# Kernel tuning notes

Measured on AMD Instinct MI355X. Metric: run time of the kernel, lower is better.

The kernel has to match this reference:

```python
import jax, jax.numpy as jnp
import numpy as np

N_NODES = 100000
N_EDGES = 1600000
IN_DIM, HID, OUT = 256, 128, 32


def setup_inputs() -> dict:
    key = jax.random.key(0)
    ks = jax.random.split(key, 8)
    x = jax.random.normal(ks[0], (N_NODES, IN_DIM), dtype=jnp.float32)
    edge_index = jax.random.randint(ks[1], (2, N_EDGES), 0, N_NODES, dtype=jnp.int64)
    # Glorot-ish small scale to keep activations stable
    W0 = jax.random.normal(ks[2], (IN_DIM, HID), dtype=jnp.float32) * 0.05
    W1 = jax.random.normal(ks[3], (HID, HID), dtype=jnp.float32) * 0.05
    W2 = jax.random.normal(ks[4], (HID, OUT), dtype=jnp.float32) * 0.05
    b0 = jnp.zeros((HID,), jnp.float32)
    b1 = jnp.zeros((HID,), jnp.float32)
    b2 = jnp.zeros((OUT,), jnp.float32)
    return {"x": x, "edge_index": edge_index, "W0": W0, "b0": b0,
            "W1": W1, "b1": b1, "W2": W2, "b2": b2}


def reference(x, edge_index, W0, b0, W1, b1, W2, b2):
    # PyG GCNConv: add self-loops, symmetric normalization D^-1/2 A D^-1/2,
    # messages flow src (row 0) -> dst (row 1), aggregated at dst.
    n = x.shape[0]
    src, dst = edge_index[0], edge_index[1]
    ones = jnp.ones((src.shape[0],), x.dtype)
    deg = jax.ops.segment_sum(ones, dst, num_segments=n) + 1.0  # +1 for self-loop
    dinv = jax.lax.rsqrt(deg)                                   # [N]
    edge_norm = dinv[src] * dinv[dst]                           # [E]
    self_norm = dinv * dinv                                     # [N] self-loop weight

    def gcn_conv(h, W, b):
        h = h @ W                                               # [N, D_out]
        agg = jax.ops.segment_sum(h[src] * edge_norm[:, None], dst, num_segments=n)
        return agg + h * self_norm[:, None] + b

    h = gcn_conv(x, W0, b0)
    # dropout after layers i != 0: identity in eval mode (deterministic reference)
    h = gcn_conv(h, W1, b1)
    h = gcn_conv(h, W2, b2)
    return jax.nn.log_softmax(h, axis=1)
```

## Files before the change

kernel.cpp:

```cpp
#include <hip/hip_runtime.h>
#include <hip/hip_bf16.h>
#include <type_traits>

#define N_NODES 100000
#define N_EDGES 1600000
#define SLICE_N 12500
#define CAP     64

typedef float f32x4 __attribute__((ext_vector_type(4)));
typedef _Float16 f16x8 __attribute__((ext_vector_type(8)));
typedef _Float16 f16x4 __attribute__((ext_vector_type(4)));

__global__ __launch_bounds__(256) void fill_bucket_kernel(const int* __restrict__ esrc,
                                                          const int* __restrict__ edst,
                                                          int* __restrict__ cnt,
                                                          int* __restrict__ esorted) {
    const int slice = blockIdx.x & 7;
    const int chunk = blockIdx.x >> 3;
    const int base = chunk * 2048 + threadIdx.x;
    const int lo = slice * SLICE_N, hi = lo + SLICE_N;
    #pragma unroll
    for (int i = 0; i < 8; ++i) {
        int e = base + i * 256;
        if (e < N_EDGES) {
            int d = edst[e];
            if (d >= lo && d < hi) {
                int pos = atomicAdd(&cnt[d], 1);
                if (pos < CAP) esorted[(size_t)d * CAP + pos] = esrc[e];
            }
        }
    }
}

__global__ void dinv_kernel(const int* __restrict__ cnt, float* __restrict__ dinv) {
    int i = blockIdx.x * 256 + threadIdx.x;
    if (i < N_NODES) dinv[i] = 1.0f / sqrtf((float)cnt[i] + 1.0f);
}

__global__ void wconv_all_kernel(const float* __restrict__ W0, const float* __restrict__ W1,
                                 const float* __restrict__ W2, _Float16* __restrict__ Wt0,
                                 _Float16* __restrict__ Wt1, _Float16* __restrict__ Wt2) {
    int i = blockIdx.x * 256 + threadIdx.x;
    if (i < 32768) {
        int k = i / 128, col = i % 128;
        Wt0[col * 256 + k] = (_Float16)W0[i];
    } else if (i < 49152) {
        int j = i - 32768;
        int k = j / 128, col = j % 128;
        Wt1[col * 128 + k] = (_Float16)W1[j];
    } else if (i < 53248) {
        int j = i - 49152;
        int k = j / 32, col = j % 32;
        Wt2[col * 128 + k] = (_Float16)W2[j];
    }
}

#define LOADA(st, k0)                                                          \
    do {                                                                       \
        _Pragma("unroll")                                                      \
        for (int r = 0; r < 2; ++r) {                                          \
            const AT* ap = A + (size_t)gr[r] * K + (k0) + kof;                 \
            if constexpr (AF32) {                                              \
                a32[st][r][0] = *(const f32x4*)ap;                             \
                a32[st][r][1] = *(const f32x4*)(ap + 4);                       \
            } else {                                                           \
                a16[st][r] = *(const f16x8*)ap;                                \
            }                                                                  \
        }                                                                      \
    } while (0)

#define LOADB(st, k0)                                                          \
    do {                                                                       \
        _Pragma("unroll")                                                      \
        for (int c = 0; c < FC; ++c)                                           \
            bst[st][c] = *(const f16x8*)(Bt + (size_t)(c * 16 + l15) * K + (k0) + kof); \
    } while (0)

template<int K, int M, typename AT>
__global__ __launch_bounds__(256) void mfma_gemm_f16(const AT* __restrict__ A,
                                                     const _Float16* __restrict__ Bt,
                                                     const float* __restrict__ dinv,
                                                     _Float16* __restrict__ C) {
    constexpr bool AF32 = std::is_same<AT, float>::value;
    constexpr int FC = M / 16;
    constexpr int NIT = K / 32;
    const int tid = threadIdx.x;
    const int wave = tid >> 6, lane = tid & 63;
    const int row0 = blockIdx.x * 128;
    const int r0 = wave * 32;
    const int l15 = lane & 15, kof = (lane >> 4) * 8;

    f32x4 acc[2][FC] = {};
    int gr[2];
    #pragma unroll
    for (int r = 0; r < 2; ++r) {
        int g = row0 + r0 + r * 16 + l15;
        gr[r] = (g < N_NODES) ? g : N_NODES - 1;
    }

    f32x4 a32[3][2][2];
    f16x8 a16[3][2];
    f16x8 bst[2][FC];

    LOADA(0, 0);
    if (NIT > 1) LOADA(1, 32);
    LOADB(0, 0);

    #pragma unroll
    for (int it = 0; it < NIT; ++it) {
        if (it + 2 < NIT) LOADA((it + 2) % 3, (it + 2) * 32);
        if (it + 1 < NIT) LOADB((it + 1) % 2, (it + 1) * 32);
        f16x8 af[2];
        #pragma unroll
        for (int r = 0; r < 2; ++r) {
            if constexpr (AF32) {
                #pragma unroll
                for (int j = 0; j < 4; ++j) {
                    af[r][j] = (_Float16)a32[it % 3][r][0][j];
                    af[r][4 + j] = (_Float16)a32[it % 3][r][1][j];
                }
            } else {
                af[r] = a16[it % 3][r];
            }
        }
        #pragma unroll
        for (int c = 0; c < FC; ++c)
            #pragma unroll
            for (int r = 0; r < 2; ++r)
                acc[r][c] = __builtin_amdgcn_mfma_f32_16x16x32_f16(af[r], bst[it % 2][c], acc[r][c], 0, 0, 0);
    }

    #pragma unroll
    for (int r = 0; r < 2; ++r) {
        #pragma unroll
        for (int j = 0; j < 4; ++j) {
            int g = row0 + r0 + r * 16 + (lane >> 4) * 4 + j;
            if (g >= N_NODES) continue;
            float s = dinv[g];
            #pragma unroll
            for (int c = 0; c < FC; ++c)
                C[(size_t)g * M + c * 16 + l15] = (_Float16)(acc[r][c][j] * s);
        }
    }
}

template<int M, int G>
__global__ __launch_bounds__(256) void gather_kernel(const int* __restrict__ cnt,
                                                     const int* __restrict__ esorted,
                                                     const float* __restrict__ dinv,
                                                     const f16x8* __restrict__ hs,
                                                     const float* __restrict__ bias,
                                                     _Float16* __restrict__ out) {
    static_assert(M == 8 * G, "layout");
    constexpr int R = M / 8;
    int gid = blockIdx.x * blockDim.x + threadIdx.x;
    int node = gid / G;
    int lane = gid % G;
    if (node >= N_NODES) return;
    int len = cnt[node]; if (len > CAP) len = CAP;
    const int* __restrict__ lst = esorted + (size_t)node * CAP;
    float dn = dinv[node];
    f16x8 hv = hs[(size_t)node * R + lane];
    float acc[8];
    #pragma unroll
    for (int d = 0; d < 8; ++d) acc[d] = (float)hv[d];
    int j = 0;
    for (; j + 8 <= len; j += 8) {
        int s[8];
        f16x8 v[8];
        #pragma unroll
        for (int k = 0; k < 8; ++k) s[k] = lst[j + k];
        #pragma unroll
        for (int k = 0; k < 8; ++k) v[k] = hs[(size_t)s[k] * R + lane];
        #pragma unroll
        for (int k = 0; k < 8; ++k)
            #pragma unroll
            for (int d = 0; d < 8; ++d) acc[d] += (float)v[k][d];
    }
    for (; j < len; ++j) {
        f16x8 v = hs[(size_t)lst[j] * R + lane];
        #pragma unroll
        for (int d = 0; d < 8; ++d) acc[d] += (float)v[d];
    }
    const float* bp = bias + lane * 8;
    f16x8 o;
    #pragma unroll
    for (int d = 0; d < 8; ++d) o[d] = (_Float16)(acc[d] * dn + bp[d]);
    *((f16x8*)out + (size_t)node * R + lane) = o;
}

__global__ __launch_bounds__(256) void gather_lsm_kernel(const int* __restrict__ cnt,
                                                         const int* __restrict__ esorted,
                                                         const float* __restrict__ dinv,
                                                         const f16x8* __restrict__ hs,
                                                         const float* __restrict__ bias,
                                                         float* __restrict__ out) {
    constexpr int R = 4;
    int gid = blockIdx.x * blockDim.x + threadIdx.x;
    int node = gid / 4;
    int lane = gid % 4;
    if (node >= N_NODES) return;
    int len = cnt[node]; if (len > CAP) len = CAP;
    const int* __restrict__ lst = esorted + (size_t)node * CAP;
    float dn = dinv[node];
    f16x8 hv = hs[(size_t)node * R + lane];
    float acc[8];
    #pragma unroll
    for (int d = 0; d < 8; ++d) acc[d] = (float)hv[d];
    int j = 0;
    for (; j + 8 <= len; j += 8) {
        int s[8];
        f16x8 v[8];
        #pragma unroll
        for (int k = 0; k < 8; ++k) s[k] = lst[j + k];
        #pragma unroll
        for (int k = 0; k < 8; ++k) v[k] = hs[(size_t)s[k] * R + lane];
        #pragma unroll
        for (int k = 0; k < 8; ++k)
            #pragma unroll
            for (int d = 0; d < 8; ++d) acc[d] += (float)v[k][d];
    }
    for (; j < len; ++j) {
        f16x8 v = hs[(size_t)lst[j] * R + lane];
        #pragma unroll
        for (int d = 0; d < 8; ++d) acc[d] += (float)v[d];
    }
    const float* bp = bias + lane * 8;
    float o[8];
    #pragma unroll
    for (int d = 0; d < 8; ++d) o[d] = acc[d] * dn + bp[d];
    float m = o[0];
    #pragma unroll
    for (int d = 1; d < 8; ++d) m = fmaxf(m, o[d]);
    m = fmaxf(m, __shfl_xor(m, 1, 4));
    m = fmaxf(m, __shfl_xor(m, 2, 4));
    float s = 0.f;
    #pragma unroll
    for (int d = 0; d < 8; ++d) s += expf(o[d] - m);
    s += __shfl_xor(s, 1, 4);
    s += __shfl_xor(s, 2, 4);
    float ls = m + logf(s);
    f32x4 r0, r1;
    #pragma unroll
    for (int d = 0; d < 4; ++d) { r0[d] = o[d] - ls; r1[d] = o[4 + d] - ls; }
    f32x4* op = (f32x4*)out + (size_t)node * 8 + lane * 2;
    op[0] = r0;
    op[1] = r1;
}

extern "C" void kernel_launch(void* const* d_in, const int* in_sizes, int n_in,
                              void* d_out, int out_size, void* d_ws, size_t ws_size,
                              hipStream_t stream) {
    const float* x  = (const float*)d_in[0];
    const int*   ei = (const int*)d_in[1];
    const float* W0 = (const float*)d_in[2];
    const float* b0 = (const float*)d_in[3];
    const float* W1 = (const float*)d_in[4];
    const float* b1 = (const float*)d_in[5];
    const float* W2 = (const float*)d_in[6];
    const float* b2 = (const float*)d_in[7];
    float* out = (float*)d_out;

    char* ws = (char*)d_ws;
    float* dinv    = (float*)(ws + 0);
    int*   cnt     = (int*)  (ws + (512 << 10));
    int*   esorted = (int*)  (ws + (1 << 20));
    _Float16* Wt0  = (_Float16*)(ws + 27262976);
    _Float16* Wt1  = (_Float16*)(ws + 27262976 + 65536);
    _Float16* Wt2  = (_Float16*)(ws + 27262976 + 98304);
    _Float16* hs     = (_Float16*)(ws + 28311552);
    _Float16* bufB16 = (_Float16*)(ws + 28311552 + 26214400);
    const int* esrc = ei;
    const int* edst = ei + N_EDGES;

    const int NB = (N_NODES + 255) / 256;

    (void)hipMemsetAsync(cnt, 0, N_NODES * sizeof(int), stream);
    {
        const int chunks = (N_EDGES + 2047) / 2048;
        fill_bucket_kernel<<<chunks * 8, 256, 0, stream>>>(esrc, edst, cnt, esorted);
    }
    dinv_kernel<<<NB, 256, 0, stream>>>(cnt, dinv);
    wconv_all_kernel<<<208, 256, 0, stream>>>(W0, W1, W2, Wt0, Wt1, Wt2);

    const int RB128 = (N_NODES + 127) / 128;

    mfma_gemm_f16<256, 128, float><<<RB128, 256, 0, stream>>>(x, Wt0, dinv, hs);
    gather_kernel<128, 16><<<(N_NODES * 16 + 255) / 256, 256, 0, stream>>>(
        cnt, esorted, dinv, (const f16x8*)hs, b0, bufB16);

    mfma_gemm_f16<128, 128, _Float16><<<RB128, 256, 0, stream>>>(bufB16, Wt1, dinv, hs);
    gather_kernel<128, 16><<<(N_NODES * 16 + 255) / 256, 256, 0, stream>>>(
        cnt, esorted, dinv, (const f16x8*)hs, b1, bufB16);

    mfma_gemm_f16<128, 32, _Float16><<<RB128, 256, 0, stream>>>(bufB16, Wt2, dinv, hs);
    gather_lsm_kernel<<<(N_NODES * 4 + 255) / 256, 256, 0, stream>>>(
        cnt, esorted, dinv, (const f16x8*)hs, b2, out);
}
```

Measured before the change: 336.7 us.

## Co-schedule edge bucketing with first GEMM in one launch, defer dinv scaling

The edge-bucketing fill and the first layer's GEMM now run in a single launch, with one GEMM block interleaved among every eight fill blocks. The goal is to overlap the atomic-heavy, latency-bound bucketing with the bandwidth-bound x·W0 multiply. Because the degree counts are not final while the GEMM runs, the GEMM writes unscaled output. A new kernel then computes dinv and rescales hs in place, which replaces the old dinv kernel. The cost is an extra full read and write of the fp16 hidden buffer, plus added rounding from scaling after the fp16 store.

New measurement: 330.7 us. No clear change (-1.8%).

```diff
diff --git a/kernel.cpp b/kernel.cpp
--- a/kernel.cpp
+++ b/kernel.cpp
@@ -10,32 +10,6 @@
 typedef float f32x4 __attribute__((ext_vector_type(4)));
 typedef _Float16 f16x8 __attribute__((ext_vector_type(8)));
 typedef _Float16 f16x4 __attribute__((ext_vector_type(4)));
-
-__global__ __launch_bounds__(256) void fill_bucket_kernel(const int* __restrict__ esrc,
-                                                          const int* __restrict__ edst,
-                                                          int* __restrict__ cnt,
-                                                          int* __restrict__ esorted) {
-    const int slice = blockIdx.x & 7;
-    const int chunk = blockIdx.x >> 3;
-    const int base = chunk * 2048 + threadIdx.x;
-    const int lo = slice * SLICE_N, hi = lo + SLICE_N;
-    #pragma unroll
-    for (int i = 0; i < 8; ++i) {
-        int e = base + i * 256;
-        if (e < N_EDGES) {
-            int d = edst[e];
-            if (d >= lo && d < hi) {
-                int pos = atomicAdd(&cnt[d], 1);
-                if (pos < CAP) esorted[(size_t)d * CAP + pos] = esrc[e];
-            }
-        }
-    }
-}
-
-__global__ void dinv_kernel(const int* __restrict__ cnt, float* __restrict__ dinv) {
-    int i = blockIdx.x * 256 + threadIdx.x;
-    if (i < N_NODES) dinv[i] = 1.0f / sqrtf((float)cnt[i] + 1.0f);
-}
 
 __global__ void wconv_all_kernel(const float* __restrict__ W0, const float* __restrict__ W1,
                                  const float* __restrict__ W2, _Float16* __restrict__ Wt0,
@@ -76,17 +50,17 @@
             bst[st][c] = *(const f16x8*)(Bt + (size_t)(c * 16 + l15) * K + (k0) + kof); \
     } while (0)
 
-template<int K, int M, typename AT>
-__global__ __launch_bounds__(256) void mfma_gemm_f16(const AT* __restrict__ A,
-                                                     const _Float16* __restrict__ Bt,
-                                                     const float* __restrict__ dinv,
-                                                     _Float16* __restrict__ C) {
+template<int K, int M, typename AT, bool SCALE>
+__device__ __forceinline__ void gemm_tile_body(const AT* __restrict__ A,
+                                               const _Float16* __restrict__ Bt,
+                                               const float* __restrict__ dinv,
+                                               _Float16* __restrict__ C,
+                                               int blk, int tid) {
     constexpr bool AF32 = std::is_same<AT, float>::value;
     constexpr int FC = M / 16;
     constexpr int NIT = K / 32;
-    const int tid = threadIdx.x;
     const int wave = tid >> 6, lane = tid & 63;
-    const int row0 = blockIdx.x * 128;
+    const int row0 = blk * 128;
     const int r0 = wave * 32;
     const int l15 = lane & 15, kof = (lane >> 4) * 8;
 
@@ -136,12 +110,65 @@
         for (int j = 0; j < 4; ++j) {
             int g = row0 + r0 + r * 16 + (lane >> 4) * 4 + j;
             if (g >= N_NODES) continue;
-            float s = dinv[g];
+            float s = SCALE ? dinv[g] : 1.0f;
             #pragma unroll
             for (int c = 0; c < FC; ++c)
                 C[(size_t)g * M + c * 16 + l15] = (_Float16)(acc[r][c][j] * s);
         }
     }
+}
+
+template<int K, int M, typename AT>
+__global__ __launch_bounds__(256) void mfma_gemm_f16(const AT* __restrict__ A,
+                                                     const _Float16* __restrict__ Bt,
+                                                     const float* __restrict__ dinv,
+                                                     _Float16* __restrict__ C) {
+    gemm_tile_body<K, M, AT, true>(A, Bt, dinv, C, blockIdx.x, threadIdx.x);
+}
+
+__global__ __launch_bounds__(256) void fused_fill_gemm0(const int* __restrict__ esrc,
+                                                        const int* __restrict__ edst,
+                                                        int* __restrict__ cnt,
+                                                        int* __restrict__ esorted,
+                                                        const float* __restrict__ x,
+                                                        const _Float16* __restrict__ Wt0,
+                                                        _Float16* __restrict__ h) {
+    const int b = blockIdx.x;
+    const int g = b / 9;
+    if (b % 9 == 0) {
+        gemm_tile_body<256, 128, float, false>(x, Wt0, nullptr, h, g, threadIdx.x);
+        return;
+    }
+    const int f = b - g - 1;
+    const int slice = b & 7;
+    const int chunk = f >> 3;
+    const int base = chunk * 2048 + threadIdx.x;
+    const int lo = slice * SLICE_N, hi = lo + SLICE_N;
+    #pragma unroll
+    for (int i = 0; i < 8; ++i) {
+        int e = base + i * 256;
+        if (e < N_EDGES) {
+            int d = edst[e];
+            if (d >= lo && d < hi) {
+                int pos = atomicAdd(&cnt[d], 1);
+                if (pos < CAP) esorted[(size_t)d * CAP + pos] = esrc[e];
+            }
+        }
+    }
+}
+
+__global__ __launch_bounds__(256) void scale_dinv_kernel(const int* __restrict__ cnt,
+                                                         float* __restrict__ dinv,
+                                                         f16x8* __restrict__ hs) {
+    int i = blockIdx.x * 256 + threadIdx.x;
+    if (i >= N_NODES * 16) return;
+    int n = i >> 4;
+    float dn = 1.0f / sqrtf((float)cnt[n] + 1.0f);
+    if ((i & 15) == 0) dinv[n] = dn;
+    f16x8 v = hs[i];
+    #pragma unroll
+    for (int d = 0; d < 8; ++d) v[d] = (_Float16)((float)v[d] * dn);
+    hs[i] = v;
 }
 
 template<int M, int G>
@@ -273,19 +300,13 @@
     const int* esrc = ei;
     const int* edst = ei + N_EDGES;
 
-    const int NB = (N_NODES + 255) / 256;
-
     (void)hipMemsetAsync(cnt, 0, N_NODES * sizeof(int), stream);
-    {
-        const int chunks = (N_EDGES + 2047) / 2048;
-        fill_bucket_kernel<<<chunks * 8, 256, 0, stream>>>(esrc, edst, cnt, esorted);
-    }
-    dinv_kernel<<<NB, 256, 0, stream>>>(cnt, dinv);
     wconv_all_kernel<<<208, 256, 0, stream>>>(W0, W1, W2, Wt0, Wt1, Wt2);
+    fused_fill_gemm0<<<782 * 9, 256, 0, stream>>>(esrc, edst, cnt, esorted, x, Wt0, hs);
+    scale_dinv_kernel<<<(N_NODES * 16) / 256, 256, 0, stream>>>(cnt, dinv, (f16x8*)hs);
 
     const int RB128 = (N_NODES + 127) / 128;
 
-    mfma_gemm_f16<256, 128, float><<<RB128, 256, 0, stream>>>(x, Wt0, dinv, hs);
     gather_kernel<128, 16><<<(N_NODES * 16 + 255) / 256, 256, 0, stream>>>(
         cnt, esorted, dinv, (const f16x8*)hs, b0, bufB16);
 
```
